# Kernel optimization log

Hardware: AMD Instinct MI355X
Metric: run time of the kernel (lower is better)

The kernel has to match this reference:

```python
import jax, jax.numpy as jnp
import numpy as np
import math

B, S, D, H = 2, 2048, 1024, 16
HD = D // H            # head dim = 64
E, K = 8, 2            # routed experts, top-k
HM = 1024              # moe_inter_dim (multiple_of=256 keeps it)
HS = 1024              # shared expert hidden = moe_inter_dim * n_shared_experts
EPS = 1e-6
TEMP = 1.0


def setup_inputs() -> dict:
    key = jax.random.key(0)
    ks = jax.random.split(key, 16)
    s = 0.02
    x = jax.random.normal(ks[0], (B, S, D), jnp.float32)
    # RoPE angles: theta = 10000
    inv_freq = 1.0 / (10000.0 ** (np.arange(0, HD, 2, dtype=np.float32) / HD))  # (HD//2,)
    ang = np.arange(S, dtype=np.float32)[:, None] * inv_freq[None, :]           # (S, HD//2)
    freqs_cos = jnp.asarray(np.cos(ang))
    freqs_sin = jnp.asarray(np.sin(ang))
    return {
        "x": x,
        "freqs_cos": freqs_cos,
        "freqs_sin": freqs_sin,
        "att_norm_w": jnp.ones((D,), jnp.float32),
        "ffn_norm_w": jnp.ones((D,), jnp.float32),
        "wq": jax.random.normal(ks[1], (D, D), jnp.float32) * s,
        "wk": jax.random.normal(ks[2], (D, D), jnp.float32) * s,
        "wv": jax.random.normal(ks[3], (D, D), jnp.float32) * s,
        "wo": jax.random.normal(ks[4], (D, D), jnp.float32) * s,
        "gate_w": jax.random.normal(ks[5], (E, D), jnp.float32) * s,
        "ew1": jax.random.normal(ks[6], (E, D, HM), jnp.float32) * s,
        "ew2": jax.random.normal(ks[7], (E, HM, D), jnp.float32) * s,
        "ew3": jax.random.normal(ks[8], (E, D, HM), jnp.float32) * s,
        "sw1": jax.random.normal(ks[9], (D, HS), jnp.float32) * s,
        "sw2": jax.random.normal(ks[10], (HS, D), jnp.float32) * s,
        "sw3": jax.random.normal(ks[11], (D, HS), jnp.float32) * s,
    }


def _rmsnorm(x, w):
    return x * jax.lax.rsqrt(jnp.mean(x * x, axis=-1, keepdims=True) + EPS) * w


def _rope(t, cos, sin):
    # t: (B,H,S,HD); rotate pairs (even, odd) like complex multiply
    tr = t.reshape(B, H, S, HD // 2, 2)
    t0, t1 = tr[..., 0], tr[..., 1]
    c = cos[None, None, :, :]
    s_ = sin[None, None, :, :]
    o0 = t0 * c - t1 * s_
    o1 = t0 * s_ + t1 * c
    return jnp.stack([o0, o1], axis=-1).reshape(B, H, S, HD)


def reference(x, freqs_cos, freqs_sin, att_norm_w, ffn_norm_w,
              wq, wk, wv, wo, gate_w, ew1, ew2, ew3, sw1, sw2, sw3):
    # ---- attention sub-block ----
    xn = _rmsnorm(x, att_norm_w)
    q = (xn @ wq).reshape(B, S, H, HD).transpose(0, 2, 1, 3)  # (B,H,S,HD)
    k = (xn @ wk).reshape(B, S, H, HD).transpose(0, 2, 1, 3)
    v = (xn @ wv).reshape(B, S, H, HD).transpose(0, 2, 1, 3)
    q = _rope(q, freqs_cos, freqs_sin)
    k = _rope(k, freqs_cos, freqs_sin)
    scores = jnp.einsum('bhqd,bhkd->bhqk', q, k) / math.sqrt(HD)
    attn = jax.nn.softmax(scores, axis=-1)
    out = jnp.einsum('bhqk,bhkd->bhqd', attn, v)
    out = out.transpose(0, 2, 1, 3).reshape(B, S, D) @ wo
    h = x + out

    # ---- MoE sub-block ----
    xf = _rmsnorm(h, ffn_norm_w).reshape(-1, D)  # (N,D), N=B*S
    # shared expert (SwiGLU)
    shared = (jax.nn.silu(xf @ sw1) * (xf @ sw3)) @ sw2
    # gate (eval mode: no noise)
    g_scores = (xf @ gate_w.T) / TEMP
    probs = jax.nn.softmax(g_scores, axis=-1)          # (N,E)
    vals, idx = jax.lax.top_k(probs, K)                 # (N,K)
    vals = vals / (jnp.sum(vals, axis=-1, keepdims=True) + 1e-9)
    # per-token per-expert weight (equivalent to scatter into expert_mask)
    mask = jnp.sum(jax.nn.one_hot(idx, E, dtype=xf.dtype) * vals[..., None], axis=1)  # (N,E)
    # routed experts: dense per-expert SwiGLU, weighted combine (zero weight => no contribution)
    h1 = jax.nn.silu(jnp.einsum('nd,edh->enh', xf, ew1)) * jnp.einsum('nd,edh->enh', xf, ew3)
    eo = jnp.einsum('enh,ehd->end', h1, ew2)            # (E,N,D)
    y = jnp.einsum('end,ne->nd', eo, mask) + shared
    return h + y.reshape(B, S, D)
```

## Files before the change

kernel.cpp:

```cpp
#include <hip/hip_runtime.h>
#include <hip/hip_bf16.h>
#include <stdint.h>


typedef __hip_bfloat16 bf16;
typedef __attribute__((ext_vector_type(8))) __bf16 bf16x8;
typedef __attribute__((ext_vector_type(4))) float f32x4;
typedef __attribute__((ext_vector_type(16))) float f32x16;
typedef __attribute__((ext_vector_type(2))) unsigned int u32x2;

#define S_  2048
#define D_  1024
#define N_  4096

__device__ __forceinline__ float b2f(bf16 h) { return __bfloat162float(h); }
__device__ __forceinline__ bf16  f2b(float f) { return __float2bfloat16(f); }

__device__ __forceinline__ bf16x8 ld_bf16x8(const bf16* p) {
    union { uint4 u; bf16x8 v; } x;
    x.u = *(const uint4*)p;
    return x.v;
}

__device__ __forceinline__ void gload_lds16(const void* gsrc, void* ldst) {
    __builtin_amdgcn_global_load_lds(
        (__attribute__((address_space(1))) void*)const_cast<void*>(gsrc),
        (__attribute__((address_space(3))) void*)ldst, 16, 0, 0);
}

__device__ __forceinline__ u32x2 tr16_read(unsigned lds_off) {
    u32x2 d;
    asm volatile("ds_read_b64_tr_b16 %0, %1" : "=v"(d) : "v"(lds_off));
    return d;
}

__device__ __forceinline__ int swz4(int r) { return ((r >> 1) ^ (r >> 3)) & 3; }

__global__ __launch_bounds__(256)
void transpose_all(const float* __restrict__ wq, const float* __restrict__ wk,
                   const float* __restrict__ wv, const float* __restrict__ wo,
                   const float* __restrict__ ew1, const float* __restrict__ ew2,
                   const float* __restrict__ ew3, const float* __restrict__ sw1,
                   const float* __restrict__ sw2, const float* __restrict__ sw3,
                   bf16* __restrict__ wqkv_t, bf16* __restrict__ wo_t,
                   bf16* __restrict__ ew13_t, bf16* __restrict__ ew2_t)
{
    __shared__ float t[64][65];
    const int z = blockIdx.z;
    const float* in; bf16* out; int rm = 1, ro = 0;
    if (z < 3)        { in = (z == 0 ? wq : z == 1 ? wk : wv); out = wqkv_t + (size_t)z * 1048576; }
    else if (z == 3)  { in = wo; out = wo_t; }
    else if (z < 12)  { const int e = z - 4;  in = ew1 + (size_t)e * 1048576; out = ew13_t + (size_t)e * 2097152; rm = 2; ro = 0; }
    else if (z < 20)  { const int e = z - 12; in = ew3 + (size_t)e * 1048576; out = ew13_t + (size_t)e * 2097152; rm = 2; ro = 1; }
    else if (z < 28)  { const int e = z - 20; in = ew2 + (size_t)e * 1048576; out = ew2_t + (size_t)e * 1048576; }
    else if (z == 28) { in = sw1; out = ew13_t + (size_t)8 * 2097152; rm = 2; ro = 0; }
    else if (z == 29) { in = sw3; out = ew13_t + (size_t)8 * 2097152; rm = 2; ro = 1; }
    else              { in = sw2; out = ew2_t + (size_t)8 * 1048576; }

    const int c0 = blockIdx.x * 64, r0 = blockIdx.y * 64;
    const int tx = (threadIdx.x & 15) * 4, ty = threadIdx.x >> 4;
#pragma unroll
    for (int i = 0; i < 4; i++)
        *(float4*)&t[ty + i * 16][tx] = *(const float4*)(in + (size_t)(r0 + ty + i * 16) * 1024 + c0 + tx);
    __syncthreads();
#pragma unroll
    for (int i = 0; i < 4; i++) {
        const int lc = ty + i * 16;
        union { bf16 h[4]; uint2 u; } pk;
#pragma unroll
        for (int j = 0; j < 4; j++) pk.h[j] = f2b(t[tx + j][lc]);
        *(uint2*)&out[(size_t)((c0 + lc) * rm + ro) * 1024 + r0 + tx] = pk.u;
    }
}

__global__ __launch_bounds__(256)
void rmsnorm_kernel(const float* __restrict__ x, const float* __restrict__ w,
                    bf16* __restrict__ out)
{
    const int n = blockIdx.x;
    const int tid = threadIdx.x;
    const float4 v = *(const float4*)(x + (size_t)n * D_ + tid * 4);
    float ss = v.x * v.x + v.y * v.y + v.z * v.z + v.w * v.w;
#pragma unroll
    for (int m = 1; m < 64; m <<= 1) ss += __shfl_xor(ss, m);
    __shared__ float red[4];
    if ((tid & 63) == 0) red[tid >> 6] = ss;
    __syncthreads();
    const float tot = red[0] + red[1] + red[2] + red[3];
    const float rstd = rsqrtf(tot * (1.0f / D_) + 1e-6f);
    const float4 wv = *(const float4*)(w + tid * 4);
    union { bf16 h[4]; uint2 u; } pk;
    pk.h[0] = f2b(v.x * rstd * wv.x);
    pk.h[1] = f2b(v.y * rstd * wv.y);
    pk.h[2] = f2b(v.z * rstd * wv.z);
    pk.h[3] = f2b(v.w * rstd * wv.w);
    *(uint2*)(out + (size_t)n * D_ + tid * 4) = pk.u;
}

template<int EPI, int MODE>
__global__ __launch_bounds__(256)
void gemm_bt(const bf16* __restrict__ A, const bf16* __restrict__ Bt,
             void* __restrict__ Cout, const float* __restrict__ resid,
             int M, int Kdim, int lda, int ldb, int ldc, long bstride,
             const int* __restrict__ tlist, const int* __restrict__ offs,
             const float* __restrict__ fc, const float* __restrict__ fs)
{
    __shared__ bf16 As[2][128 * 32];
    __shared__ bf16 Bs[2][128 * 32];
    const int tid = threadIdx.x;
    const int wave = tid >> 6, lane = tid & 63;

    int bx, by;
    if constexpr (MODE == 0) {
        const int gx = gridDim.x;
        const int nwg = gx * gridDim.y;
        int flat = blockIdx.y * gx + blockIdx.x;
        flat = (flat & 7) * (nwg >> 3) + (flat >> 3);
        bx = flat % gx; by = flat / gx;
    } else {
        bx = blockIdx.x; by = blockIdx.y;
    }

    int mcount = M, outBase = 0;
    const bf16* Bp = Bt;
    if (MODE != 0) {
        const int e = blockIdx.z;
        outBase = offs[e];
        mcount = offs[e + 1] - outBase;
        Bp = Bt + (size_t)e * bstride;
    }
    const int m0 = by * 128;
    if (m0 >= mcount) return;
    const int n0 = bx * 128;

    const int srow = tid >> 2;
    const int sc4 = tid & 3;
    const int scol = (sc4 ^ swz4(srow)) * 8;
    const bf16* aptr[2];
    const bf16* bptr[2];
#pragma unroll
    for (int i = 0; i < 2; i++) {
        int r = m0 + i * 64 + srow;
        if (r >= mcount) r = mcount - 1;
        long arow;
        if (MODE == 1)      arow = tlist[outBase + r];
        else if (MODE == 2) arow = (long)outBase + r;
        else                arow = r;
        aptr[i] = A + (size_t)arow * lda + scol;
        bptr[i] = Bp + (size_t)(n0 + i * 64 + srow) * ldb + scol;
    }

    f32x16 acc[2][2];
#pragma unroll
    for (int tm = 0; tm < 2; tm++)
#pragma unroll
        for (int tn = 0; tn < 2; tn++)
#pragma unroll
            for (int i = 0; i < 16; i++) acc[tm][tn][i] = 0.f;

    const int wm = (wave >> 1) * 64, wn = (wave & 1) * 64;
    const int l31 = lane & 31, l5 = lane >> 5;

    int aoff[2][2], boff[2][2];
#pragma unroll
    for (int tm = 0; tm < 2; tm++) {
        const int ra = wm + tm * 32 + l31;
        const int rb = wn + tm * 32 + l31;
#pragma unroll
        for (int kk = 0; kk < 2; kk++) {
            const int g = kk * 2 + l5;
            aoff[tm][kk] = ra * 32 + (g ^ swz4(ra)) * 8;
            boff[tm][kk] = rb * 32 + (g ^ swz4(rb)) * 8;
        }
    }

    const int nkt = Kdim >> 5;
#pragma unroll
    for (int i = 0; i < 2; i++) {
        gload_lds16(aptr[i], (char*)&As[0][0] + i * 4096 + wave * 1024);
        gload_lds16(bptr[i], (char*)&Bs[0][0] + i * 4096 + wave * 1024);
    }

    int p = 0;
    for (int kt = 0; kt < nkt; kt++) {
        if (kt + 1 < nkt) {
            const int ko = (kt + 1) << 5;
#pragma unroll
            for (int i = 0; i < 2; i++) {
                gload_lds16(aptr[i] + ko, (char*)&As[p ^ 1][0] + i * 4096 + wave * 1024);
                gload_lds16(bptr[i] + ko, (char*)&Bs[p ^ 1][0] + i * 4096 + wave * 1024);
            }
            asm volatile("s_waitcnt vmcnt(4)" ::: "memory");
        } else {
            asm volatile("s_waitcnt vmcnt(0)" ::: "memory");
        }
        asm volatile("s_barrier" ::: "memory");

        const bf16* Ab = &As[p][0];
        const bf16* Bb = &Bs[p][0];
#pragma unroll
        for (int kk = 0; kk < 2; kk++) {
            bf16x8 af[2], bfr[2];
#pragma unroll
            for (int tm = 0; tm < 2; tm++) af[tm] = ld_bf16x8(&Ab[aoff[tm][kk]]);
#pragma unroll
            for (int tn = 0; tn < 2; tn++) bfr[tn] = ld_bf16x8(&Bb[boff[tn][kk]]);
#pragma unroll
            for (int tm = 0; tm < 2; tm++)
#pragma unroll
                for (int tn = 0; tn < 2; tn++)
                    acc[tm][tn] = __builtin_amdgcn_mfma_f32_32x32x16_bf16(af[tm], bfr[tn], acc[tm][tn], 0, 0, 0);
        }

        asm volatile("s_barrier" ::: "memory");
        p ^= 1;
    }

#pragma unroll
    for (int tm = 0; tm < 2; tm++)
#pragma unroll
        for (int tn = 0; tn < 2; tn++)
#pragma unroll
            for (int i = 0; i < 16; i++) {
                const int r = m0 + wm + tm * 32 + (i & 3) + 8 * (i >> 2) + 4 * l5;
                const int c = n0 + wn + tn * 32 + l31;
                const float v = acc[tm][tn][i];
                if (EPI == 3) {
                    const float other = __shfl_xor(v, 1);
                    const float res = (v / (1.f + __expf(-v))) * other;
                    if (((lane & 1) == 0) && r < mcount)
                        ((bf16*)Cout)[(size_t)(outBase + r) * ldc + (c >> 1)] = f2b(res);
                } else if (EPI == 4) {
                    const float other = __shfl_xor(v, 1);
                    float o = v;
                    if (c < 2048) {
                        const int s = r & (S_ - 1);
                        const int jf = (c & 63) >> 1;
                        const float co = fc[s * 32 + jf], si = fs[s * 32 + jf];
                        o = v * co + other * ((c & 1) ? si : -si);
                        if (c < 1024) o *= 0.125f;
                    }
                    ((bf16*)Cout)[(size_t)r * ldc + c] = f2b(o);
                } else if (r < mcount) {
                    const size_t oi = (size_t)(outBase + r) * ldc + c;
                    if (EPI == 0)      ((bf16*)Cout)[oi] = f2b(v);
                    else if (EPI == 1) ((float*)Cout)[oi] = v;
                    else               ((float*)Cout)[oi] = resid[oi] + v;
                }
            }
}

__global__ __launch_bounds__(256)
void attn_kernel(const bf16* __restrict__ qkv, bf16* __restrict__ out)
{
    __shared__ __align__(16) bf16 Ks[64 * 72];
    __shared__ __align__(16) bf16 Vs[4 * 1032 + 8];
    const int tid = threadIdx.x, wave = tid >> 6, lane = tid & 63;
    const int b = blockIdx.z, hh = blockIdx.y;
    const int q0 = blockIdx.x * 128;
    const bf16* base  = qkv + ((size_t)b * S_) * 3072 + (size_t)hh * 64;
    const bf16* kbase = base + 1024;
    const bf16* vbase = base + 2048;
    const int fr = lane & 15, fg = lane >> 4;

    bf16x8 aq[2][2];
#pragma unroll
    for (int qb = 0; qb < 2; qb++)
#pragma unroll
        for (int s2 = 0; s2 < 2; s2++)
            aq[qb][s2] = ld_bf16x8(base + (size_t)(q0 + wave * 32 + qb * 16 + fr) * 3072 + s2 * 32 + fg * 8);

    f32x4 zero4 = {0.f, 0.f, 0.f, 0.f};
    f32x4 acc_o[2][4];
    float mrow[2], lrow[2];
#pragma unroll
    for (int qb = 0; qb < 2; qb++) {
#pragma unroll
        for (int hf = 0; hf < 4; hf++) acc_o[qb][hf] = zero4;
        mrow[qb] = -1e30f; lrow[qb] = 0.f;
    }

    const int srow = tid >> 2, sc4 = tid & 3;
    const unsigned vtr0 =
        (unsigned)(uintptr_t)(__attribute__((address_space(3))) void*)&Vs[0] + lane * 8;

    uint4 kg0, kg1, vg0, vg1;
    {
        const bf16* kr = kbase + (size_t)srow * 3072 + sc4 * 16;
        kg0 = *(const uint4*)kr; kg1 = *(const uint4*)(kr + 8);
        const bf16* vr = vbase + (size_t)srow * 3072 + sc4 * 16;
        vg0 = *(const uint4*)vr; vg1 = *(const uint4*)(vr + 8);
    }

    for (int kv0 = 0; kv0 < S_; kv0 += 64) {
        __syncthreads();
        *(uint4*)&Ks[srow * 72 + sc4 * 16]         = kg0;
        *(uint4*)&Ks[srow * 72 + sc4 * 16 + 8]     = kg1;
        *(uint4*)&Vs[sc4 * 1032 + srow * 16]       = vg0;
        *(uint4*)&Vs[sc4 * 1032 + srow * 16 + 8]   = vg1;
        __syncthreads();
        if (kv0 + 64 < S_) {
            const bf16* kr = kbase + (size_t)(kv0 + 64 + srow) * 3072 + sc4 * 16;
            kg0 = *(const uint4*)kr; kg1 = *(const uint4*)(kr + 8);
            const bf16* vr = vbase + (size_t)(kv0 + 64 + srow) * 3072 + sc4 * 16;
            vg0 = *(const uint4*)vr; vg1 = *(const uint4*)(vr + 8);
        }

        f32x4 sc[4][2];
#pragma unroll
        for (int kt = 0; kt < 4; kt++)
#pragma unroll
            for (int qb = 0; qb < 2; qb++) sc[kt][qb] = zero4;
        __builtin_amdgcn_s_setprio(1);
#pragma unroll
        for (int kt = 0; kt < 4; kt++) {
            const bf16x8 k0 = ld_bf16x8(&Ks[(kt * 16 + fr) * 72 + fg * 8]);
            const bf16x8 k1 = ld_bf16x8(&Ks[(kt * 16 + fr) * 72 + 32 + fg * 8]);
#pragma unroll
            for (int qb = 0; qb < 2; qb++) {
                sc[kt][qb] = __builtin_amdgcn_mfma_f32_16x16x32_bf16(k0, aq[qb][0], sc[kt][qb], 0, 0, 0);
                sc[kt][qb] = __builtin_amdgcn_mfma_f32_16x16x32_bf16(k1, aq[qb][1], sc[kt][qb], 0, 0, 0);
            }
        }
        __builtin_amdgcn_s_setprio(0);

        bf16x8 pcomb[2][2];
        float scalv[2];
#pragma unroll
        for (int qb = 0; qb < 2; qb++) {
            float pm = -1e30f;
#pragma unroll
            for (int kt = 0; kt < 4; kt++)
#pragma unroll
                for (int j = 0; j < 4; j++) pm = fmaxf(pm, sc[kt][qb][j]);
            pm = fmaxf(pm, __shfl_xor(pm, 16));
            pm = fmaxf(pm, __shfl_xor(pm, 32));
            const float mnew = fmaxf(mrow[qb], pm);
            const float scal = __expf(mrow[qb] - mnew);
            mrow[qb] = mnew;
            float ps = 0.f;
            union { bf16 h[16]; bf16x8 v8[2]; } pk;
#pragma unroll
            for (int kt = 0; kt < 4; kt++)
#pragma unroll
                for (int j = 0; j < 4; j++) {
                    const float p = __expf(sc[kt][qb][j] - mnew);
                    ps += p;
                    pk.h[kt * 4 + j] = f2b(p);
                }
            pcomb[qb][0] = pk.v8[0];
            pcomb[qb][1] = pk.v8[1];
            ps += __shfl_xor(ps, 16);
            ps += __shfl_xor(ps, 32);
            lrow[qb] = lrow[qb] * scal + ps;
            scalv[qb] = scal;
        }

#pragma unroll
        for (int j = 0; j < 4; j++) {
            const int src = (lane & 48) + fg * 4 + j;
            const float s0 = __shfl(scalv[0], src);
            const float s1 = __shfl(scalv[1], src);
#pragma unroll
            for (int hf = 0; hf < 4; hf++) {
                acc_o[0][hf][j] *= s0;
                acc_o[1][hf][j] *= s1;
            }
        }

#pragma unroll
        for (int tp = 0; tp < 2; tp++) {
            union { u32x2 d2[2]; bf16x8 v8; } vc[4];
#pragma unroll
            for (int hf = 0; hf < 4; hf++) {
                vc[hf].d2[0] = tr16_read(vtr0 + hf * 2064 + (tp * 2)     * 512);
                vc[hf].d2[1] = tr16_read(vtr0 + hf * 2064 + (tp * 2 + 1) * 512);
            }
            asm volatile("s_waitcnt lgkmcnt(0)" ::: "memory");
            __builtin_amdgcn_sched_barrier(0);
            __builtin_amdgcn_s_setprio(1);
#pragma unroll
            for (int hf = 0; hf < 4; hf++)
#pragma unroll
                for (int qb = 0; qb < 2; qb++)
                    acc_o[qb][hf] = __builtin_amdgcn_mfma_f32_16x16x32_bf16(
                        pcomb[qb][tp], vc[hf].v8, acc_o[qb][hf], 0, 0, 0);
            __builtin_amdgcn_s_setprio(0);
        }
    }

#pragma unroll
    for (int qb = 0; qb < 2; qb++) {
        const float inv = 1.f / lrow[qb];
#pragma unroll
        for (int j = 0; j < 4; j++) {
            const float ij = __shfl(inv, (lane & 48) + fg * 4 + j);
            const int r = q0 + wave * 32 + qb * 16 + fg * 4 + j;
#pragma unroll
            for (int hf = 0; hf < 4; hf++)
                out[((size_t)(b * S_ + r)) * D_ + hh * 64 + hf * 16 + fr] =
                    f2b(acc_o[qb][hf][j] * ij);
        }
    }
}

__global__ __launch_bounds__(256)
void gating_kernel(const float* __restrict__ h, const float* __restrict__ gw,
                   const float* __restrict__ wnorm,
                   int* __restrict__ top_idx, float* __restrict__ top_w)
{
    const int wave = threadIdx.x >> 6, lane = threadIdx.x & 63;
    const int n = blockIdx.x * 4 + wave;
    const float* hr = h + (size_t)n * D_;
    float acc[8] = {0.f, 0.f, 0.f, 0.f, 0.f, 0.f, 0.f, 0.f};
    float ss = 0.f;
    for (int d = lane * 4; d < D_; d += 256) {
        const float4 hv = *(const float4*)(hr + d);
        const float4 wv = *(const float4*)(wnorm + d);
        ss += hv.x * hv.x + hv.y * hv.y + hv.z * hv.z + hv.w * hv.w;
        const float x0 = hv.x * wv.x, x1 = hv.y * wv.y, x2 = hv.z * wv.z, x3 = hv.w * wv.w;
#pragma unroll
        for (int e2 = 0; e2 < 8; e2++) {
            const float4 gv = *(const float4*)(gw + e2 * D_ + d);
            acc[e2] += x0 * gv.x + x1 * gv.y + x2 * gv.z + x3 * gv.w;
        }
    }
#pragma unroll
    for (int m = 1; m < 64; m <<= 1) {
        ss += __shfl_xor(ss, m);
#pragma unroll
        for (int e2 = 0; e2 < 8; e2++) acc[e2] += __shfl_xor(acc[e2], m);
    }
    if (lane == 0) {
        const float rstd = rsqrtf(ss * (1.0f / D_) + 1e-6f);
        float s[8];
#pragma unroll
        for (int e2 = 0; e2 < 8; e2++) s[e2] = acc[e2] * rstd;
        int e0 = 0;
#pragma unroll
        for (int e2 = 1; e2 < 8; e2++) if (s[e2] > s[e0]) e0 = e2;
        int e1 = (e0 == 0) ? 1 : 0;
#pragma unroll
        for (int e2 = 0; e2 < 8; e2++) if (e2 != e0 && s[e2] > s[e1]) e1 = e2;
        const float mx = s[e0];
        float Z = 0.f;
        float p[8];
#pragma unroll
        for (int e2 = 0; e2 < 8; e2++) { p[e2] = __expf(s[e2] - mx); Z += p[e2]; }
        const float v0 = p[e0] / Z, v1 = p[e1] / Z;
        const float sm = v0 + v1 + 1e-9f;
        top_idx[n * 2] = e0; top_idx[n * 2 + 1] = e1;
        top_w[n * 2] = v0 / sm; top_w[n * 2 + 1] = v1 / sm;
    }
}

__global__ __launch_bounds__(1024)
void route_kernel(const int* __restrict__ top_idx, int* __restrict__ offs,
                  int* __restrict__ token_list, int* __restrict__ tok_pos)
{
    __shared__ int hist[8];
    __shared__ int base[8];
    const int tid = threadIdx.x;
    if (tid < 8) hist[tid] = 0;
    __syncthreads();
    int4 e4a = *(const int4*)(top_idx + tid * 8);
    int4 e4b = *(const int4*)(top_idx + tid * 8 + 4);
    int myidx[8] = {e4a.x, e4a.y, e4a.z, e4a.w, e4b.x, e4b.y, e4b.z, e4b.w};
#pragma unroll
    for (int i = 0; i < 8; i++) atomicAdd(&hist[myidx[i]], 1);
    __syncthreads();
    if (tid == 0) {
        int o = 0;
#pragma unroll
        for (int e = 0; e < 8; e++) { base[e] = o; offs[e] = o; o += hist[e]; }
        offs[8] = o;
        offs[9] = o + N_;
    }
    __syncthreads();
    if (tid < 8) hist[tid] = 0;
    __syncthreads();
#pragma unroll
    for (int i = 0; i < 8; i++) {
        const int entry = tid * 8 + i;
        const int e = myidx[i];
        const int pos = base[e] + atomicAdd(&hist[e], 1);
        token_list[pos] = entry >> 1;
        tok_pos[entry] = pos;
    }
#pragma unroll
    for (int i = 0; i < 4; i++)
        token_list[2 * N_ + tid * 4 + i] = tid * 4 + i;
}

__global__ __launch_bounds__(256)
void combine_kernel(const float* __restrict__ h, const bf16* __restrict__ eo,
                    const int* __restrict__ tok_pos, const float* __restrict__ top_w,
                    float* __restrict__ out)
{
    const int idx = blockIdx.x * 256 + threadIdx.x;
    const int n = idx >> 8;
    const int c = (idx & 255) * 4;
    const float4 hv = *(const float4*)(h + (size_t)n * D_ + c);
    const int p0 = tok_pos[n * 2], p1 = tok_pos[n * 2 + 1];
    const float w0 = top_w[n * 2], w1 = top_w[n * 2 + 1];
    union { uint2 u; bf16 hh[4]; } a0, a1, ash;
    a0.u  = *(const uint2*)(eo + (size_t)p0 * D_ + c);
    a1.u  = *(const uint2*)(eo + (size_t)p1 * D_ + c);
    ash.u = *(const uint2*)(eo + (size_t)(2 * N_ + n) * D_ + c);
    float4 r;
    r.x = hv.x + b2f(ash.hh[0]) + w0 * b2f(a0.hh[0]) + w1 * b2f(a1.hh[0]);
    r.y = hv.y + b2f(ash.hh[1]) + w0 * b2f(a0.hh[1]) + w1 * b2f(a1.hh[1]);
    r.z = hv.z + b2f(ash.hh[2]) + w0 * b2f(a0.hh[2]) + w1 * b2f(a1.hh[2]);
    r.w = hv.w + b2f(ash.hh[3]) + w0 * b2f(a0.hh[3]) + w1 * b2f(a1.hh[3]);
    *(float4*)(out + (size_t)n * D_ + c) = r;
}

extern "C" void kernel_launch(void* const* d_in, const int* in_sizes, int n_in,
                              void* d_out, int out_size, void* d_ws, size_t ws_size,
                              hipStream_t stream)
{
    const float* x   = (const float*)d_in[0];
    const float* fc  = (const float*)d_in[1];
    const float* fs  = (const float*)d_in[2];
    const float* anw = (const float*)d_in[3];
    const float* fnw = (const float*)d_in[4];
    const float* wq  = (const float*)d_in[5];
    const float* wk  = (const float*)d_in[6];
    const float* wv  = (const float*)d_in[7];
    const float* wo  = (const float*)d_in[8];
    const float* gw  = (const float*)d_in[9];
    const float* ew1 = (const float*)d_in[10];
    const float* ew2 = (const float*)d_in[11];
    const float* ew3 = (const float*)d_in[12];
    const float* sw1 = (const float*)d_in[13];
    const float* sw2 = (const float*)d_in[14];
    const float* sw3 = (const float*)d_in[15];

    char* ws = (char*)d_ws;
    bf16*  wqkv_t = (bf16*)(ws + 0);
    bf16*  wo_t   = (bf16*)(ws + 6291456);
    bf16*  ew13_t = (bf16*)(ws + 8388608);
    bf16*  ew2_t  = (bf16*)(ws + 46137344);
    bf16*  xn     = (bf16*)(ws + 65011712);
    bf16*  qkv    = (bf16*)(ws + 73400320);
    bf16*  attn   = (bf16*)(ws + 98566144);
    float* hbuf   = (float*)(ws + 106954752);
    bf16*  eo     = (bf16*)(ws + 123731968);
    char*  misc   = ws + 148897792;
    int*   offs       = (int*)(misc + 0);
    int*   top_idx    = (int*)(misc + 128);
    float* top_w      = (float*)(misc + 128 + 32768);
    int*   token_list = (int*)(misc + 128 + 65536);
    int*   tok_pos    = (int*)(misc + 128 + 131072);

    const dim3 tb(256);
    transpose_all<<<dim3(16, 16, 31), tb, 0, stream>>>(
        wq, wk, wv, wo, ew1, ew2, ew3, sw1, sw2, sw3,
        wqkv_t, wo_t, ew13_t, ew2_t);

    rmsnorm_kernel<<<N_, tb, 0, stream>>>(x, anw, xn);
    gemm_bt<4, 0><<<dim3(24, 32, 1), tb, 0, stream>>>(xn, wqkv_t, qkv, nullptr,
        N_, 1024, 1024, 1024, 3072, 0, nullptr, nullptr, fc, fs);
    attn_kernel<<<dim3(16, 16, 2), tb, 0, stream>>>(qkv, attn);
    gemm_bt<2, 0><<<dim3(8, 32, 1), tb, 0, stream>>>(attn, wo_t, hbuf, x,
        N_, 1024, 1024, 1024, 1024, 0, nullptr, nullptr, nullptr, nullptr);

    rmsnorm_kernel<<<N_, tb, 0, stream>>>(hbuf, fnw, xn);
    gating_kernel<<<N_ / 4, tb, 0, stream>>>(hbuf, gw, fnw, top_idx, top_w);
    route_kernel<<<1, 1024, 0, stream>>>(top_idx, offs, token_list, tok_pos);

    gemm_bt<3, 1><<<dim3(16, 32, 9), tb, 0, stream>>>(xn, ew13_t, qkv, nullptr,
        0, 1024, 1024, 1024, 1024, 2097152, token_list, offs, nullptr, nullptr);
    gemm_bt<0, 2><<<dim3(8, 32, 9), tb, 0, stream>>>((const bf16*)qkv, ew2_t, eo, nullptr,
        0, 1024, 1024, 1024, 1024, 1048576, nullptr, offs, nullptr, nullptr);

    combine_kernel<<<4096, tb, 0, stream>>>(hbuf, eo, tok_pos, top_w, (float*)d_out);
}
```

Baseline: 399.1 us.

## Use 512-thread GEMM blocks with eight waves each computing a 64x32 sub-tile

The 128x128 GEMM tile is now split across eight waves instead of four. Each wave holds two 32x32 accumulators rather than four, and each thread issues one A and one B global-to-LDS load per k-step instead of two. The aim is more waves per CU and fewer accumulator registers per thread, to hide latency better. The cost is more barrier participants, a lower MFMA-to-LDS-read ratio per wave (three fragment reads per two MFMAs instead of four per four), and possible LDS bank pressure.

```diff
diff --git a/kernel.cpp b/kernel.cpp
--- a/kernel.cpp
+++ b/kernel.cpp
@@ -98,7 +98,7 @@
 }
 
 template<int EPI, int MODE>
-__global__ __launch_bounds__(256)
+__global__ __launch_bounds__(512)
 void gemm_bt(const bf16* __restrict__ A, const bf16* __restrict__ Bt,
              void* __restrict__ Cout, const float* __restrict__ resid,
              int M, int Kdim, int lda, int ldb, int ldc, long bstride,
@@ -136,61 +136,50 @@
     const int srow = tid >> 2;
     const int sc4 = tid & 3;
     const int scol = (sc4 ^ swz4(srow)) * 8;
-    const bf16* aptr[2];
-    const bf16* bptr[2];
-#pragma unroll
-    for (int i = 0; i < 2; i++) {
-        int r = m0 + i * 64 + srow;
-        if (r >= mcount) r = mcount - 1;
-        long arow;
-        if (MODE == 1)      arow = tlist[outBase + r];
-        else if (MODE == 2) arow = (long)outBase + r;
-        else                arow = r;
-        aptr[i] = A + (size_t)arow * lda + scol;
-        bptr[i] = Bp + (size_t)(n0 + i * 64 + srow) * ldb + scol;
-    }
-
-    f32x16 acc[2][2];
+    int rA = m0 + srow;
+    if (rA >= mcount) rA = mcount - 1;
+    long arow;
+    if (MODE == 1)      arow = tlist[outBase + rA];
+    else if (MODE == 2) arow = (long)outBase + rA;
+    else                arow = rA;
+    const bf16* aptr = A + (size_t)arow * lda + scol;
+    const bf16* bptr = Bp + (size_t)(n0 + srow) * ldb + scol;
+
+    f32x16 acc[2];
 #pragma unroll
     for (int tm = 0; tm < 2; tm++)
 #pragma unroll
-        for (int tn = 0; tn < 2; tn++)
-#pragma unroll
-            for (int i = 0; i < 16; i++) acc[tm][tn][i] = 0.f;
-
-    const int wm = (wave >> 1) * 64, wn = (wave & 1) * 64;
+        for (int i = 0; i < 16; i++) acc[tm][i] = 0.f;
+
+    const int wm = (wave >> 2) * 64, wn = (wave & 3) * 32;
     const int l31 = lane & 31, l5 = lane >> 5;
 
-    int aoff[2][2], boff[2][2];
+    int aoff[2][2], boff[2];
 #pragma unroll
     for (int tm = 0; tm < 2; tm++) {
         const int ra = wm + tm * 32 + l31;
-        const int rb = wn + tm * 32 + l31;
-#pragma unroll
-        for (int kk = 0; kk < 2; kk++) {
-            const int g = kk * 2 + l5;
-            aoff[tm][kk] = ra * 32 + (g ^ swz4(ra)) * 8;
-            boff[tm][kk] = rb * 32 + (g ^ swz4(rb)) * 8;
-        }
+#pragma unroll
+        for (int kk = 0; kk < 2; kk++)
+            aoff[tm][kk] = ra * 32 + ((kk * 2 + l5) ^ swz4(ra)) * 8;
+    }
+    {
+        const int rb = wn + l31;
+#pragma unroll
+        for (int kk = 0; kk < 2; kk++)
+            boff[kk] = rb * 32 + ((kk * 2 + l5) ^ swz4(rb)) * 8;
     }
 
     const int nkt = Kdim >> 5;
-#pragma unroll
-    for (int i = 0; i < 2; i++) {
-        gload_lds16(aptr[i], (char*)&As[0][0] + i * 4096 + wave * 1024);
-        gload_lds16(bptr[i], (char*)&Bs[0][0] + i * 4096 + wave * 1024);
-    }
+    gload_lds16(aptr, (char*)&As[0][0] + wave * 1024);
+    gload_lds16(bptr, (char*)&Bs[0][0] + wave * 1024);
 
     int p = 0;
     for (int kt = 0; kt < nkt; kt++) {
         if (kt + 1 < nkt) {
             const int ko = (kt + 1) << 5;
-#pragma unroll
-            for (int i = 0; i < 2; i++) {
-                gload_lds16(aptr[i] + ko, (char*)&As[p ^ 1][0] + i * 4096 + wave * 1024);
-                gload_lds16(bptr[i] + ko, (char*)&Bs[p ^ 1][0] + i * 4096 + wave * 1024);
-            }
-            asm volatile("s_waitcnt vmcnt(4)" ::: "memory");
+            gload_lds16(aptr + ko, (char*)&As[p ^ 1][0] + wave * 1024);
+            gload_lds16(bptr + ko, (char*)&Bs[p ^ 1][0] + wave * 1024);
+            asm volatile("s_waitcnt vmcnt(2)" ::: "memory");
         } else {
             asm volatile("s_waitcnt vmcnt(0)" ::: "memory");
         }
@@ -200,16 +189,11 @@
         const bf16* Bb = &Bs[p][0];
 #pragma unroll
         for (int kk = 0; kk < 2; kk++) {
-            bf16x8 af[2], bfr[2];
-#pragma unroll
-            for (int tm = 0; tm < 2; tm++) af[tm] = ld_bf16x8(&Ab[aoff[tm][kk]]);
-#pragma unroll
-            for (int tn = 0; tn < 2; tn++) bfr[tn] = ld_bf16x8(&Bb[boff[tn][kk]]);
-#pragma unroll
-            for (int tm = 0; tm < 2; tm++)
-#pragma unroll
-                for (int tn = 0; tn < 2; tn++)
-                    acc[tm][tn] = __builtin_amdgcn_mfma_f32_32x32x16_bf16(af[tm], bfr[tn], acc[tm][tn], 0, 0, 0);
+            const bf16x8 bf0 = ld_bf16x8(&Bb[boff[kk]]);
+            const bf16x8 af0 = ld_bf16x8(&Ab[aoff[0][kk]]);
+            const bf16x8 af1 = ld_bf16x8(&Ab[aoff[1][kk]]);
+            acc[0] = __builtin_amdgcn_mfma_f32_32x32x16_bf16(af0, bf0, acc[0], 0, 0, 0);
+            acc[1] = __builtin_amdgcn_mfma_f32_32x32x16_bf16(af1, bf0, acc[1], 0, 0, 0);
         }
 
         asm volatile("s_barrier" ::: "memory");
@@ -219,35 +203,33 @@
 #pragma unroll
     for (int tm = 0; tm < 2; tm++)
 #pragma unroll
-        for (int tn = 0; tn < 2; tn++)
-#pragma unroll
-            for (int i = 0; i < 16; i++) {
-                const int r = m0 + wm + tm * 32 + (i & 3) + 8 * (i >> 2) + 4 * l5;
-                const int c = n0 + wn + tn * 32 + l31;
-                const float v = acc[tm][tn][i];
-                if (EPI == 3) {
-                    const float other = __shfl_xor(v, 1);
-                    const float res = (v / (1.f + __expf(-v))) * other;
-                    if (((lane & 1) == 0) && r < mcount)
-                        ((bf16*)Cout)[(size_t)(outBase + r) * ldc + (c >> 1)] = f2b(res);
-                } else if (EPI == 4) {
-                    const float other = __shfl_xor(v, 1);
-                    float o = v;
-                    if (c < 2048) {
-                        const int s = r & (S_ - 1);
-                        const int jf = (c & 63) >> 1;
-                        const float co = fc[s * 32 + jf], si = fs[s * 32 + jf];
-                        o = v * co + other * ((c & 1) ? si : -si);
-                        if (c < 1024) o *= 0.125f;
-                    }
-                    ((bf16*)Cout)[(size_t)r * ldc + c] = f2b(o);
-                } else if (r < mcount) {
-                    const size_t oi = (size_t)(outBase + r) * ldc + c;
-                    if (EPI == 0)      ((bf16*)Cout)[oi] = f2b(v);
-                    else if (EPI == 1) ((float*)Cout)[oi] = v;
-                    else               ((float*)Cout)[oi] = resid[oi] + v;
+        for (int i = 0; i < 16; i++) {
+            const int r = m0 + wm + tm * 32 + (i & 3) + 8 * (i >> 2) + 4 * l5;
+            const int c = n0 + wn + l31;
+            const float v = acc[tm][i];
+            if (EPI == 3) {
+                const float other = __shfl_xor(v, 1);
+                const float res = (v / (1.f + __expf(-v))) * other;
+                if (((lane & 1) == 0) && r < mcount)
+                    ((bf16*)Cout)[(size_t)(outBase + r) * ldc + (c >> 1)] = f2b(res);
+            } else if (EPI == 4) {
+                const float other = __shfl_xor(v, 1);
+                float o = v;
+                if (c < 2048) {
+                    const int s = r & (S_ - 1);
+                    const int jf = (c & 63) >> 1;
+                    const float co = fc[s * 32 + jf], si = fs[s * 32 + jf];
+                    o = v * co + other * ((c & 1) ? si : -si);
+                    if (c < 1024) o *= 0.125f;
                 }
+                ((bf16*)Cout)[(size_t)r * ldc + c] = f2b(o);
+            } else if (r < mcount) {
+                const size_t oi = (size_t)(outBase + r) * ldc + c;
+                if (EPI == 0)      ((bf16*)Cout)[oi] = f2b(v);
+                else if (EPI == 1) ((float*)Cout)[oi] = v;
+                else               ((float*)Cout)[oi] = resid[oi] + v;
             }
+        }
 }
 
 __global__ __launch_bounds__(256)
@@ -554,24 +536,25 @@
     int*   tok_pos    = (int*)(misc + 128 + 131072);
 
     const dim3 tb(256);
+    const dim3 tb512(512);
     transpose_all<<<dim3(16, 16, 31), tb, 0, stream>>>(
         wq, wk, wv, wo, ew1, ew2, ew3, sw1, sw2, sw3,
         wqkv_t, wo_t, ew13_t, ew2_t);
 
     rmsnorm_kernel<<<N_, tb, 0, stream>>>(x, anw, xn);
-    gemm_bt<4, 0><<<dim3(24, 32, 1), tb, 0, stream>>>(xn, wqkv_t, qkv, nullptr,
+    gemm_bt<4, 0><<<dim3(24, 32, 1), tb512, 0, stream>>>(xn, wqkv_t, qkv, nullptr,
         N_, 1024, 1024, 1024, 3072, 0, nullptr, nullptr, fc, fs);
     attn_kernel<<<dim3(16, 16, 2), tb, 0, stream>>>(qkv, attn);
-    gemm_bt<2, 0><<<dim3(8, 32, 1), tb, 0, stream>>>(attn, wo_t, hbuf, x,
+    gemm_bt<2, 0><<<dim3(8, 32, 1), tb512, 0, stream>>>(attn, wo_t, hbuf, x,
         N_, 1024, 1024, 1024, 1024, 0, nullptr, nullptr, nullptr, nullptr);
 
     rmsnorm_kernel<<<N_, tb, 0, stream>>>(hbuf, fnw, xn);
     gating_kernel<<<N_ / 4, tb, 0, stream>>>(hbuf, gw, fnw, top_idx, top_w);
     route_kernel<<<1, 1024, 0, stream>>>(top_idx, offs, token_list, tok_pos);
 
-    gemm_bt<3, 1><<<dim3(16, 32, 9), tb, 0, stream>>>(xn, ew13_t, qkv, nullptr,
+    gemm_bt<3, 1><<<dim3(16, 32, 9), tb512, 0, stream>>>(xn, ew13_t, qkv, nullptr,
         0, 1024, 1024, 1024, 1024, 2097152, token_list, offs, nullptr, nullptr);
-    gemm_bt<0, 2><<<dim3(8, 32, 9), tb, 0, stream>>>((const bf16*)qkv, ew2_t, eo, nullptr,
+    gemm_bt<0, 2><<<dim3(8, 32, 9), tb512, 0, stream>>>((const bf16*)qkv, ew2_t, eo, nullptr,
         0, 1024, 1024, 1024, 1024, 1048576, nullptr, offs, nullptr, nullptr);
 
     combine_kernel<<<4096, tb, 0, stream>>>(hbuf, eo, tok_pos, top_w, (float*)d_out);
```

After: 353.7 us (median of 2 runs). 11.4% less time.
